# Performance work log

Hardware: AMD Instinct MI355X
Metric: run time of the kernel (lower is better)

## Reference

```python
import jax, jax.numpy as jnp
import numpy as np

# Problem-size constants (match input_specs / init_kwargs)
B, D, H, W = 2, 128, 128, 128   # batch and spatial grid
N = 200_000                      # number of active (non-empty) voxels
CI, CO, K = 64, 64, 3            # channels and cubic kernel size
DIL = 1                          # dilation


def setup_inputs() -> dict:
    key = jax.random.key(0)
    k1, k2, k3 = jax.random.split(key, 3)
    # Unique active voxel coordinates (submanifold conv assumes unique sites).
    rng = np.random.default_rng(0)
    lin = rng.choice(B * D * H * W, size=N, replace=False)
    b, rem = np.divmod(lin, D * H * W)
    z, rem = np.divmod(rem, H * W)
    y, x = np.divmod(rem, W)
    coords = jnp.asarray(np.stack([b, z, y, x], axis=1).astype(np.int32))  # [N,4]
    feats = jax.random.normal(k1, (N, CI), dtype=jnp.float32)
    # kaiming-uniform-ish init, layout [Co, Kd, Kh, Kw, Ci] as in the module
    fan_in = CI * K * K * K
    bound = 1.0 / np.sqrt(fan_in)
    weight = jax.random.uniform(k2, (CO, K, K, K, CI), dtype=jnp.float32,
                                minval=-bound, maxval=bound)
    bias = jax.random.uniform(k3, (CO,), dtype=jnp.float32,
                              minval=-bound, maxval=bound)
    return {"feats": feats, "weight": weight, "bias": bias, "coords": coords}


def _build_grid(coords):
    """Dense voxel hash: linear cell id -> row index in feats (-1 if empty)."""
    n = coords.shape[0]
    lin = ((coords[:, 0] * D + coords[:, 1]) * H + coords[:, 2]) * W + coords[:, 3]
    grid = jnp.full((B * D * H * W,), -1, dtype=jnp.int32)
    return grid.at[lin].set(jnp.arange(n, dtype=jnp.int32))


def reference(feats, weight, bias, coords):
    # Submanifold sparse 3D conv: out[p] = bias + sum_k W[k] @ feats[p + dil*(k - center)]
    # (only where the neighbor voxel is active; output sites == input sites).
    n = feats.shape[0]
    grid = _build_grid(coords)
    c = K // 2
    bz, z0, y0, x0 = coords[:, 0], coords[:, 1], coords[:, 2], coords[:, 3]
    out = jnp.broadcast_to(bias.astype(feats.dtype), (n, CO))
    for kd in range(K):
        for kh in range(K):
            for kw in range(K):
                dz, dy, dx = DIL * (kd - c), DIL * (kh - c), DIL * (kw - c)
                nz, ny, nx = z0 + dz, y0 + dy, x0 + dx
                inb = (nz >= 0) & (nz < D) & (ny >= 0) & (ny < H) & (nx >= 0) & (nx < W)
                nlin = ((bz * D + jnp.clip(nz, 0, D - 1)) * H
                        + jnp.clip(ny, 0, H - 1)) * W + jnp.clip(nx, 0, W - 1)
                nidx = jnp.where(inb, grid[nlin], -1)          # rulebook for this offset
                valid = (nidx >= 0)[:, None]
                g = jnp.where(valid, feats[jnp.clip(nidx, 0)], 0.0)  # gather [N,Ci]
                out = out + jnp.einsum('nc,oc->no', g, weight[:, kd, kh, kw, :])
    return out
```

## Files before the change

kernel.cpp:

```cpp
#include <hip/hip_runtime.h>
#include <hip/hip_bf16.h>

#define BDIM 2
#define DDIM 128
#define HDIM 128
#define WDIM 128
#define CI 64
#define CO 64
#define NTAPS 27
#define GRID_CELLS (BDIM * DDIM * HDIM * WDIM)
#define NCBLK (GRID_CELLS / 256)

typedef __attribute__((ext_vector_type(8))) short short8;
typedef __attribute__((ext_vector_type(4))) float floatx4;

#define WT_OFF   ((size_t)16 << 20)
#define BCNT_OFF (WT_OFF + ((size_t)256 << 10))
#define ORD_OFF  (BCNT_OFF + ((size_t)64 << 10))
#define ZROW_OFF (ORD_OFF + ((size_t)1 << 20))
#define FB_OFF   ((size_t)18 << 20)

typedef const __attribute__((address_space(1))) void* gas_t;
typedef __attribute__((address_space(3))) void* las_t;

__device__ __forceinline__ unsigned short f2bf(float f) {
    unsigned int u = __float_as_uint(f);
    return (unsigned short)((u + 0x7FFFu + ((u >> 16) & 1u)) >> 16);
}

__global__ __launch_bounds__(256) void setup_kernel(
    const int* __restrict__ coords, int* __restrict__ grid, int n,
    const float* __restrict__ weight, short8* __restrict__ wt8,
    float* __restrict__ zrow, const float* __restrict__ feats,
    short8* __restrict__ fb8, int nbf) {
    int bid = blockIdx.x, tid = threadIdx.x;
    if (bid < 54) {
        int idx = bid * 256 + tid;
        int l = idx & 63, ot = (idx >> 6) & 3, s = (idx >> 8) & 1, t = idx >> 9;
        int o = ot * 16 + (l & 15);
        int k0 = s * 32 + ((l >> 4) << 3);
        const float* src = weight + ((size_t)o * NTAPS + t) * CI + k0;
        short8 v;
#pragma unroll
        for (int j = 0; j < 8; ++j) v[j] = (short)f2bf(src[j]);
        wt8[idx] = v;
    } else if (bid == 54) {
        if (tid < 64) zrow[tid] = 0.f;
    } else if (bid < 55 + nbf) {
        int g = (bid - 55) * 256 + tid;
        if (g < n * 8) {
            const float* s = feats + (size_t)g * 8;
            short8 v;
#pragma unroll
            for (int j = 0; j < 8; ++j) v[j] = (short)f2bf(s[j]);
            fb8[g] = v;
        }
    } else {
        int i = (bid - 55 - nbf) * 256 + tid;
        if (i < n) {
            int4 c = ((const int4*)coords)[i];
            grid[((c.x * DDIM + c.y) * HDIM + c.z) * WDIM + c.w] = i;
        }
    }
}

__global__ __launch_bounds__(256) void count_kernel(
    const int* __restrict__ grid, int* __restrict__ bcnt) {
    int i = blockIdx.x * 256 + threadIdx.x;
    unsigned long long b = __ballot(grid[i] >= 0);
    __shared__ int wc[4];
    if ((threadIdx.x & 63) == 0) wc[threadIdx.x >> 6] = __popcll(b);
    __syncthreads();
    if (threadIdx.x == 0) bcnt[blockIdx.x] = wc[0] + wc[1] + wc[2] + wc[3];
}

__global__ __launch_bounds__(1024) void scan_kernel(int* __restrict__ bcnt) {
    __shared__ int part[1024];
    int tid = threadIdx.x;
    int v[16], s = 0;
#pragma unroll
    for (int k = 0; k < 16; ++k) { v[k] = bcnt[tid * 16 + k]; s += v[k]; }
    part[tid] = s;
    __syncthreads();
    for (int off = 1; off < 1024; off <<= 1) {
        int t = (tid >= off) ? part[tid - off] : 0;
        __syncthreads();
        part[tid] += t;
        __syncthreads();
    }
    int ex = tid ? part[tid - 1] : 0;
#pragma unroll
    for (int k = 0; k < 16; ++k) { int nv = ex; ex += v[k]; bcnt[tid * 16 + k] = nv; }
}

__global__ __launch_bounds__(256) void emit_kernel(
    const int* __restrict__ grid, const int* __restrict__ boff,
    int* __restrict__ order) {
    int i = blockIdx.x * 256 + threadIdx.x;
    int v = grid[i];
    int lane = threadIdx.x & 63, w = threadIdx.x >> 6;
    unsigned long long b = __ballot(v >= 0);
    __shared__ int wc[4];
    if (lane == 0) wc[w] = __popcll(b);
    __syncthreads();
    int woff = 0;
    for (int k = 0; k < w; ++k) woff += wc[k];
    if (v >= 0) {
        int rank = __popcll(b & ((1ull << lane) - 1ull));
        order[boff[blockIdx.x] + woff + rank] = v;
    }
}

template <bool BF>
__global__ __launch_bounds__(256) void conv_kernel(
    const float* __restrict__ feats, const short8* __restrict__ fb8,
    const short8* __restrict__ wt8, const float* __restrict__ bias,
    const int* __restrict__ coords, const int* __restrict__ grid,
    const int* __restrict__ order, const float* __restrict__ zrow,
    float* __restrict__ out, int n) {
    __shared__ short8 bs[4][512];
    int tid = threadIdx.x;
    int w = tid >> 6, l = tid & 63, quad = l >> 4, m = l & 15;
    int half = l >> 5, q2 = (l >> 4) & 1;

    int nwg = gridDim.x, orig = blockIdx.x;
    int q = nwg >> 3, r = nwg & 7, xcd = orig & 7;
    int bswz = (xcd < r ? xcd * (q + 1) : r * (q + 1) + (xcd - r) * q) +
               (orig >> 3);

    float b0 = bias[m], b1 = bias[m + 16], b2 = bias[m + 32], b3 = bias[m + 48];

    int jrow = bswz * 128 + w * 32 + half * 16 + m;
    int j = jrow < n ? jrow : n - 1;
    int p = order[j];
    int4 c = ((const int4*)coords)[p];

    int pr[14];
#pragma unroll
    for (int i = 0; i < 14; ++i) {
        int t = 2 * i + q2;
        int v = -1;
        if (t < NTAPS) {
            int dz = t / 9 - 1, rem = t % 9;
            int dy = rem / 3 - 1, dx = rem % 3 - 1;
            int nz = c.y + dz, ny = c.z + dy, nx = c.w + dx;
            if (nz >= 0 && nz < DDIM && ny >= 0 && ny < HDIM &&
                nx >= 0 && nx < WDIM)
                v = grid[((c.x * DDIM + nz) * HDIM + ny) * WDIM + nx];
        }
        pr[i] = v;
    }

    floatx4 acc[2][4];
#pragma unroll
    for (int a = 0; a < 2; ++a)
#pragma unroll
        for (int qq = 0; qq < 4; ++qq) acc[a][qq] = floatx4{0.f, 0.f, 0.f, 0.f};

    short8 xb[3][2][2];
    float4 xf[3][2][4];
    int vval[3][2];

#define VMW(N) asm volatile("s_waitcnt vmcnt(" #N ")" ::: "memory")

#define STAGE(t)                                                              \
    {                                                                         \
        const short8* gsrc = wt8 + (size_t)(t) * 512 + w * 128 + l;           \
        __builtin_amdgcn_global_load_lds((gas_t)gsrc,                         \
            (las_t)&bs[(t) & 3][w * 128], 16, 0, 0);                          \
        __builtin_amdgcn_global_load_lds((gas_t)(gsrc + 64),                  \
            (las_t)&bs[(t) & 3][w * 128 + 64], 16, 0, 0);                     \
    }

#define GATHER1(t, a)                                                         \
    {                                                                         \
        int vv = __shfl(pr[(t) >> 1], ((a) << 5) | (((t) & 1) << 4) | m);     \
        vval[(t) % 3][a] = vv;                                                \
        if constexpr (BF) {                                                   \
            const short8* ar =                                                \
                (vv >= 0 ? fb8 + (size_t)vv * 8 : (const short8*)zrow) + quad;\
            xb[(t) % 3][a][0] = ar[0];                                        \
            xb[(t) % 3][a][1] = ar[4];                                        \
        } else {                                                              \
            const float4* ar =                                                \
                (const float4*)(vv >= 0 ? feats + (size_t)vv * CI : zrow) +   \
                quad * 2;                                                     \
            float4* xp = xf[(t) % 3][a];                                      \
            xp[0] = ar[0]; xp[1] = ar[1]; xp[2] = ar[8]; xp[3] = ar[9];       \
        }                                                                     \
    }
#define GATHER(t) { GATHER1(t, 0); GATHER1(t, 1); }

#define COMPUTE1(t, a)                                                             \
    if (__ballot(vval[(t) % 3][a] >= 0) != 0ull) {                                 \
        short8 f0s, f1s;                                                           \
        if constexpr (BF) {                                                        \
            f0s = xb[(t) % 3][a][0];                                               \
            f1s = xb[(t) % 3][a][1];                                               \
        } else {                                                                   \
            const float4* g = xf[(t) % 3][a];                                      \
            union { short8 s; __hip_bfloat162 h[4]; } f0, f1;                      \
            f0.h[0] = __float22bfloat162_rn({g[0].x, g[0].y});                     \
            f0.h[1] = __float22bfloat162_rn({g[0].z, g[0].w});                     \
            f0.h[2] = __float22bfloat162_rn({g[1].x, g[1].y});                     \
            f0.h[3] = __float22bfloat162_rn({g[1].z, g[1].w});                     \
            f1.h[0] = __float22bfloat162_rn({g[2].x, g[2].y});                     \
            f1.h[1] = __float22bfloat162_rn({g[2].z, g[2].w});                     \
            f1.h[2] = __float22bfloat162_rn({g[3].x, g[3].y});                     \
            f1.h[3] = __float22bfloat162_rn({g[3].z, g[3].w});                     \
            f0s = f0.s; f1s = f1.s;                                                \
        }                                                                          \
        const short8* wb = &bs[(t) & 3][l];                                        \
        __builtin_amdgcn_s_setprio(1);                                             \
        acc[a][0] = __builtin_amdgcn_mfma_f32_16x16x32_bf16(f0s, wb[0 * 64], acc[a][0], 0, 0, 0); \
        acc[a][1] = __builtin_amdgcn_mfma_f32_16x16x32_bf16(f0s, wb[1 * 64], acc[a][1], 0, 0, 0); \
        acc[a][2] = __builtin_amdgcn_mfma_f32_16x16x32_bf16(f0s, wb[2 * 64], acc[a][2], 0, 0, 0); \
        acc[a][3] = __builtin_amdgcn_mfma_f32_16x16x32_bf16(f0s, wb[3 * 64], acc[a][3], 0, 0, 0); \
        acc[a][0] = __builtin_amdgcn_mfma_f32_16x16x32_bf16(f1s, wb[4 * 64], acc[a][0], 0, 0, 0); \
        acc[a][1] = __builtin_amdgcn_mfma_f32_16x16x32_bf16(f1s, wb[5 * 64], acc[a][1], 0, 0, 0); \
        acc[a][2] = __builtin_amdgcn_mfma_f32_16x16x32_bf16(f1s, wb[6 * 64], acc[a][2], 0, 0, 0); \
        acc[a][3] = __builtin_amdgcn_mfma_f32_16x16x32_bf16(f1s, wb[7 * 64], acc[a][3], 0, 0, 0); \
        __builtin_amdgcn_s_setprio(0);                                             \
    }
#define COMPUTE(t) { COMPUTE1(t, 0); COMPUTE1(t, 1); }

    STAGE(0); GATHER(0);
    STAGE(1); GATHER(1);

#pragma unroll
    for (int t = 0; t < NTAPS; ++t) {
        if (t + 2 < NTAPS) { STAGE(t + 2); GATHER(t + 2); }
        if constexpr (BF) {
            if (t < NTAPS - 2)       { VMW(12); }
            else if (t == NTAPS - 2) { VMW(6); }
            else                     { VMW(0); }
        } else {
            if (t < NTAPS - 2)       { VMW(20); }
            else if (t == NTAPS - 2) { VMW(10); }
            else                     { VMW(0); }
        }
        __builtin_amdgcn_sched_barrier(0);
        __builtin_amdgcn_s_barrier();
        __builtin_amdgcn_sched_barrier(0);
        COMPUTE(t);
        __builtin_amdgcn_sched_barrier(0);
    }

#pragma unroll
    for (int a = 0; a < 2; ++a)
#pragma unroll
        for (int rr4 = 0; rr4 < 4; ++rr4) {
            int rr = quad * 4 + rr4;
            int jr = bswz * 128 + w * 32 + a * 16 + rr;
            int prow = __shfl(p, (a << 5) | rr);
            if (jr < n) {
                float* orow = out + (size_t)prow * CO;
                orow[m]      = acc[a][0][rr4] + b0;
                orow[m + 16] = acc[a][1][rr4] + b1;
                orow[m + 32] = acc[a][2][rr4] + b2;
                orow[m + 48] = acc[a][3][rr4] + b3;
            }
        }
#undef STAGE
#undef GATHER
#undef GATHER1
#undef COMPUTE
#undef COMPUTE1
#undef VMW
}

extern "C" void kernel_launch(void* const* d_in, const int* in_sizes, int n_in,
                              void* d_out, int out_size, void* d_ws, size_t ws_size,
                              hipStream_t stream) {
    const float* feats  = (const float*)d_in[0];
    const float* weight = (const float*)d_in[1];
    const float* bias   = (const float*)d_in[2];
    const int*   coords = (const int*)d_in[3];
    float* out = (float*)d_out;
    int n = in_sizes[3] / 4;

    int*    grid  = (int*)d_ws;
    short8* wt8   = (short8*)((char*)d_ws + WT_OFF);
    int*    bcnt  = (int*)((char*)d_ws + BCNT_OFF);
    int*    order = (int*)((char*)d_ws + ORD_OFF);
    float*  zrow  = (float*)((char*)d_ws + ZROW_OFF);
    short8* fb8   = (short8*)((char*)d_ws + FB_OFF);

    int useBF = ws_size >= FB_OFF + (size_t)n * CI * 2;
    int nbf = useBF ? (n * 8 + 255) / 256 : 0;

    (void)hipMemsetAsync(grid, 0xFF, (size_t)GRID_CELLS * sizeof(int), stream);
    setup_kernel<<<55 + nbf + (n + 255) / 256, 256, 0, stream>>>(
        coords, grid, n, weight, wt8, zrow, feats, fb8, nbf);
    count_kernel<<<NCBLK, 256, 0, stream>>>(grid, bcnt);
    scan_kernel<<<1, 1024, 0, stream>>>(bcnt);
    emit_kernel<<<NCBLK, 256, 0, stream>>>(grid, bcnt, order);
    if (useBF)
        conv_kernel<true><<<(n + 127) / 128, 256, 0, stream>>>(
            feats, fb8, wt8, bias, coords, grid, order, zrow, out, n);
    else
        conv_kernel<false><<<(n + 127) / 128, 256, 0, stream>>>(
            feats, fb8, wt8, bias, coords, grid, order, zrow, out, n);
}
```

Before: 189.3 us.

## Load per-tap weights directly into registers instead of staging through LDS

Removes the LDS weight ring buffer and async global-to-LDS copies; each wave now loads the tap's weight fragments straight into registers (double-buffered) and drops the per-tap workgroup barrier. Also removes the XCD-aware block swizzle, using plain blockIdx ordering. This avoids barrier synchronization and LDS traffic, but each wave now fetches the full weight tile itself (4x redundant global/L2 reads per block), raises register pressure, and the hand-tuned vmcnt wait counts must still match the new load mix.

```diff
diff --git a/kernel.cpp b/kernel.cpp
--- a/kernel.cpp
+++ b/kernel.cpp
@@ -19,9 +19,6 @@
 #define ORD_OFF  (BCNT_OFF + ((size_t)64 << 10))
 #define ZROW_OFF (ORD_OFF + ((size_t)1 << 20))
 #define FB_OFF   ((size_t)18 << 20)
-
-typedef const __attribute__((address_space(1))) void* gas_t;
-typedef __attribute__((address_space(3))) void* las_t;
 
 __device__ __forceinline__ unsigned short f2bf(float f) {
     unsigned int u = __float_as_uint(f);
@@ -118,19 +115,13 @@
     const int* __restrict__ coords, const int* __restrict__ grid,
     const int* __restrict__ order, const float* __restrict__ zrow,
     float* __restrict__ out, int n) {
-    __shared__ short8 bs[4][512];
     int tid = threadIdx.x;
     int w = tid >> 6, l = tid & 63, quad = l >> 4, m = l & 15;
     int half = l >> 5, q2 = (l >> 4) & 1;
 
-    int nwg = gridDim.x, orig = blockIdx.x;
-    int q = nwg >> 3, r = nwg & 7, xcd = orig & 7;
-    int bswz = (xcd < r ? xcd * (q + 1) : r * (q + 1) + (xcd - r) * q) +
-               (orig >> 3);
-
     float b0 = bias[m], b1 = bias[m + 16], b2 = bias[m + 32], b3 = bias[m + 48];
 
-    int jrow = bswz * 128 + w * 32 + half * 16 + m;
+    int jrow = blockIdx.x * 128 + w * 32 + half * 16 + m;
     int j = jrow < n ? jrow : n - 1;
     int p = order[j];
     int4 c = ((const int4*)coords)[p];
@@ -157,19 +148,18 @@
 #pragma unroll
         for (int qq = 0; qq < 4; ++qq) acc[a][qq] = floatx4{0.f, 0.f, 0.f, 0.f};
 
+    short8 bw[2][8];
     short8 xb[3][2][2];
     float4 xf[3][2][4];
     int vval[3][2];
 
 #define VMW(N) asm volatile("s_waitcnt vmcnt(" #N ")" ::: "memory")
 
-#define STAGE(t)                                                              \
+#define LOADB(t)                                                              \
     {                                                                         \
-        const short8* gsrc = wt8 + (size_t)(t) * 512 + w * 128 + l;           \
-        __builtin_amdgcn_global_load_lds((gas_t)gsrc,                         \
-            (las_t)&bs[(t) & 3][w * 128], 16, 0, 0);                          \
-        __builtin_amdgcn_global_load_lds((gas_t)(gsrc + 64),                  \
-            (las_t)&bs[(t) & 3][w * 128 + 64], 16, 0, 0);                     \
+        const short8* gsrc = wt8 + (size_t)(t) * 512 + l;                     \
+        _Pragma("unroll")                                                     \
+        for (int k = 0; k < 8; ++k) bw[(t) & 1][k] = gsrc[k * 64];            \
     }
 
 #define GATHER1(t, a)                                                         \
@@ -210,40 +200,38 @@
             f1.h[3] = __float22bfloat162_rn({g[3].z, g[3].w});                     \
             f0s = f0.s; f1s = f1.s;                                                \
         }                                                                          \
-        const short8* wb = &bs[(t) & 3][l];                                        \
+        const short8* wb = bw[(t) & 1];                                            \
         __builtin_amdgcn_s_setprio(1);                                             \
-        acc[a][0] = __builtin_amdgcn_mfma_f32_16x16x32_bf16(f0s, wb[0 * 64], acc[a][0], 0, 0, 0); \
-        acc[a][1] = __builtin_amdgcn_mfma_f32_16x16x32_bf16(f0s, wb[1 * 64], acc[a][1], 0, 0, 0); \
-        acc[a][2] = __builtin_amdgcn_mfma_f32_16x16x32_bf16(f0s, wb[2 * 64], acc[a][2], 0, 0, 0); \
-        acc[a][3] = __builtin_amdgcn_mfma_f32_16x16x32_bf16(f0s, wb[3 * 64], acc[a][3], 0, 0, 0); \
-        acc[a][0] = __builtin_amdgcn_mfma_f32_16x16x32_bf16(f1s, wb[4 * 64], acc[a][0], 0, 0, 0); \
-        acc[a][1] = __builtin_amdgcn_mfma_f32_16x16x32_bf16(f1s, wb[5 * 64], acc[a][1], 0, 0, 0); \
-        acc[a][2] = __builtin_amdgcn_mfma_f32_16x16x32_bf16(f1s, wb[6 * 64], acc[a][2], 0, 0, 0); \
-        acc[a][3] = __builtin_amdgcn_mfma_f32_16x16x32_bf16(f1s, wb[7 * 64], acc[a][3], 0, 0, 0); \
+        acc[a][0] = __builtin_amdgcn_mfma_f32_16x16x32_bf16(f0s, wb[0], acc[a][0], 0, 0, 0); \
+        acc[a][1] = __builtin_amdgcn_mfma_f32_16x16x32_bf16(f0s, wb[1], acc[a][1], 0, 0, 0); \
+        acc[a][2] = __builtin_amdgcn_mfma_f32_16x16x32_bf16(f0s, wb[2], acc[a][2], 0, 0, 0); \
+        acc[a][3] = __builtin_amdgcn_mfma_f32_16x16x32_bf16(f0s, wb[3], acc[a][3], 0, 0, 0); \
+        acc[a][0] = __builtin_amdgcn_mfma_f32_16x16x32_bf16(f1s, wb[4], acc[a][0], 0, 0, 0); \
+        acc[a][1] = __builtin_amdgcn_mfma_f32_16x16x32_bf16(f1s, wb[5], acc[a][1], 0, 0, 0); \
+        acc[a][2] = __builtin_amdgcn_mfma_f32_16x16x32_bf16(f1s, wb[6], acc[a][2], 0, 0, 0); \
+        acc[a][3] = __builtin_amdgcn_mfma_f32_16x16x32_bf16(f1s, wb[7], acc[a][3], 0, 0, 0); \
         __builtin_amdgcn_s_setprio(0);                                             \
     }
 #define COMPUTE(t) { COMPUTE1(t, 0); COMPUTE1(t, 1); }
 
-    STAGE(0); GATHER(0);
-    STAGE(1); GATHER(1);
+    LOADB(0);
+    GATHER(0);
+    GATHER(1);
 
 #pragma unroll
     for (int t = 0; t < NTAPS; ++t) {
-        if (t + 2 < NTAPS) { STAGE(t + 2); GATHER(t + 2); }
+        if (t + 2 < NTAPS) { GATHER(t + 2); }
+        if (t + 1 < NTAPS) { LOADB(t + 1); }
         if constexpr (BF) {
-            if (t < NTAPS - 2)       { VMW(12); }
-            else if (t == NTAPS - 2) { VMW(6); }
+            if (t < NTAPS - 2)       { VMW(16); }
+            else if (t == NTAPS - 2) { VMW(12); }
             else                     { VMW(0); }
         } else {
-            if (t < NTAPS - 2)       { VMW(20); }
-            else if (t == NTAPS - 2) { VMW(10); }
+            if (t < NTAPS - 2)       { VMW(24); }
+            else if (t == NTAPS - 2) { VMW(16); }
             else                     { VMW(0); }
         }
-        __builtin_amdgcn_sched_barrier(0);
-        __builtin_amdgcn_s_barrier();
-        __builtin_amdgcn_sched_barrier(0);
         COMPUTE(t);
-        __builtin_amdgcn_sched_barrier(0);
     }
 
 #pragma unroll
@@ -251,7 +239,7 @@
 #pragma unroll
         for (int rr4 = 0; rr4 < 4; ++rr4) {
             int rr = quad * 4 + rr4;
-            int jr = bswz * 128 + w * 32 + a * 16 + rr;
+            int jr = blockIdx.x * 128 + w * 32 + a * 16 + rr;
             int prow = __shfl(p, (a << 5) | rr);
             if (jr < n) {
                 float* orow = out + (size_t)prow * CO;
@@ -261,7 +249,7 @@
                 orow[m + 48] = acc[a][3][rr4] + b3;
             }
         }
-#undef STAGE
+#undef LOADB
 #undef GATHER
 #undef GATHER1
 #undef COMPUTE
```

New measurement: 209.2 us. +10.5%, slower.
